# Kernel tuning notes

Hardware: AMD Instinct MI355X
Metric: run time of the kernel (lower is better)

Reference implementation:

```python
import jax, jax.numpy as jnp
import numpy as np
import math

D_MODEL = 1024
NUM_HEADS = 16
B, S = 4, 2048


def setup_inputs() -> dict:
    key = jax.random.key(0)
    ks = jax.random.split(key, 12)
    d = D_MODEL
    sc = 1.0 / math.sqrt(d)
    inp = {
        "q": jax.random.normal(ks[0], (B, S, d), jnp.float32),
        "k": jax.random.normal(ks[1], (B, S, d), jnp.float32),
        "v": jax.random.normal(ks[2], (B, S, d), jnp.float32),
        # causal mask, broadcast over batch and heads
        "mask": jnp.tril(jnp.ones((S, S), bool))[None, None, :, :],
        "Wq": jax.random.normal(ks[3], (d, d), jnp.float32) * sc,
        "bq": jnp.zeros((d,), jnp.float32),
        "Wk": jax.random.normal(ks[4], (d, d), jnp.float32) * sc,
        "bk": jnp.zeros((d,), jnp.float32),
        "Wv": jax.random.normal(ks[5], (d, d), jnp.float32) * sc,
        "bv": jnp.zeros((d,), jnp.float32),
        "Wo": jax.random.normal(ks[6], (d, d), jnp.float32) * sc,
        "bo": jnp.zeros((d,), jnp.float32),
    }
    return inp


def reference(q, k, v, mask, Wq, bq, Wk, bk, Wv, bv, Wo, bo):
    b, s, d = q.shape
    h = NUM_HEADS
    dk = d // h
    # QKV projections, then split heads: [B, H, S, dk]
    def split(x):
        return x.reshape(b, -1, h, dk).transpose(0, 2, 1, 3)
    Q = split(q @ Wq + bq)
    K = split(k @ Wk + bk)
    V = split(v @ Wv + bv)
    scores = jnp.einsum("bhqd,bhkd->bhqk", Q, K) / jnp.sqrt(jnp.float32(dk))
    scores = jnp.where(mask, scores, jnp.float32(-jnp.inf))
    attn = jax.nn.softmax(scores, axis=-1)  # dropout is identity in eval
    ctx = jnp.einsum("bhqk,bhkd->bhqd", attn, V)
    ctx = ctx.transpose(0, 2, 1, 3).reshape(b, -1, d)
    return ctx @ Wo + bo
```

## Files before the change

kernel.cpp:

```cpp
#include <hip/hip_runtime.h>
#include <hip/hip_bf16.h>

typedef unsigned short u16;
typedef __bf16 bf16x8 __attribute__((ext_vector_type(8)));
typedef float f32x4 __attribute__((ext_vector_type(4)));

#define D_MODEL 1024
#define NUM_HEADS 16
#define BATCH 4
#define SEQ 2048
#define DK 64
#define MROWS (BATCH * SEQ)
#define TENS (MROWS * D_MODEL)

#define GLOAD16(gp, lp) __builtin_amdgcn_global_load_lds( \
    (const __attribute__((address_space(1))) void*)(gp), \
    (__attribute__((address_space(3))) void*)(lp), 16, 0, 0)

__device__ inline u16 f2bf(float f) {
    __hip_bfloat16 h = __float2bfloat16(f);
    return *reinterpret_cast<u16*>(&h);
}

__global__ __launch_bounds__(256) void transpose4(
    const float* __restrict__ W0, const float* __restrict__ W1,
    const float* __restrict__ W2, const float* __restrict__ W3,
    u16* __restrict__ dst)
{
    __shared__ u16 tile[32][33];
    const float* in = (blockIdx.z == 0) ? W0 : (blockIdx.z == 1) ? W1
                    : (blockIdx.z == 2) ? W2 : W3;
    u16* out = dst + (size_t)blockIdx.z * (D_MODEL * D_MODEL);
    int x = blockIdx.x * 32 + threadIdx.x;
    int y = blockIdx.y * 32 + threadIdx.y;
    for (int i = 0; i < 32; i += 8)
        tile[threadIdx.y + i][threadIdx.x] = f2bf(in[(size_t)(y + i) * D_MODEL + x]);
    __syncthreads();
    x = blockIdx.y * 32 + threadIdx.x;
    y = blockIdx.x * 32 + threadIdx.y;
    for (int i = 0; i < 32; i += 8)
        out[(size_t)(y + i) * D_MODEL + x] = tile[threadIdx.x][threadIdx.y + i];
}

__global__ __launch_bounds__(256) void cvt_bf16(
    const float* __restrict__ x0, const float* __restrict__ x1,
    u16* __restrict__ dst)
{
    const float* x = blockIdx.z ? x1 : x0;
    u16* o = dst + (size_t)blockIdx.z * TENS;
    size_t i = ((size_t)blockIdx.x * 256 + threadIdx.x) * 8;
    f32x4 a = *(const f32x4*)(x + i);
    f32x4 b = *(const f32x4*)(x + i + 4);
    union { u16 s[8]; uint4 v; } u;
    for (int t = 0; t < 4; t++) { u.s[t] = f2bf(a[t]); u.s[4 + t] = f2bf(b[t]); }
    *(uint4*)(o + i) = u.v;
}

template<bool C_F32>
__global__ __launch_bounds__(256) void gemm_b(
    const u16* __restrict__ A0, const u16* __restrict__ A1,
    const u16* __restrict__ Bt0, const u16* __restrict__ Bt1,
    const float* __restrict__ bias0, const float* __restrict__ bias1,
    void* __restrict__ C0, void* __restrict__ C1)
{
    const int z = blockIdx.z;
    const u16* A    = z ? A1 : A0;
    const u16* Bt   = z ? Bt1 : Bt0;
    const float* bias = z ? bias1 : bias0;
    void* Cp        = z ? C1 : C0;
    const int K = D_MODEL, N = D_MODEL;

    __shared__ __align__(16) u16 As[128 * 32];
    __shared__ __align__(16) u16 Bs[128 * 32];

    const int tid  = threadIdx.x;
    const int lane = tid & 63;
    const int w    = tid >> 6;
    const int wr   = w >> 1, wc = w & 1;
    const int m0   = blockIdx.y * 128;
    const int n0   = blockIdx.x * 128;
    const int col_l = lane & 15;
    const int quad  = lane >> 4;
    const int koff  = quad * 8;

    const f32x4 fz = {0.f, 0.f, 0.f, 0.f};
    f32x4 acc[4][4];
    for (int i = 0; i < 4; i++)
        for (int j = 0; j < 4; j++) acc[i][j] = fz;

    for (int k0 = 0; k0 < K; k0 += 32) {
        __syncthreads();
        for (int i = 0; i < 2; i++) {
            int c   = w * 2 + i;
            int row = c * 16 + (lane >> 2);
            GLOAD16(A  + (size_t)(m0 + row) * K + k0 + (lane & 3) * 8, (char*)As + c * 1024);
            GLOAD16(Bt + (size_t)(n0 + row) * K + k0 + (lane & 3) * 8, (char*)Bs + c * 1024);
        }
        __syncthreads();

        bf16x8 af[4], bfr[4];
        for (int i = 0; i < 4; i++)
            af[i] = *(const bf16x8*)&As[(wr * 64 + i * 16 + col_l) * 32 + koff];
        for (int j = 0; j < 4; j++)
            bfr[j] = *(const bf16x8*)&Bs[(wc * 64 + j * 16 + col_l) * 32 + koff];
        for (int i = 0; i < 4; i++)
            for (int j = 0; j < 4; j++)
                acc[i][j] = __builtin_amdgcn_mfma_f32_16x16x32_bf16(
                    af[i], bfr[j], acc[i][j], 0, 0, 0);
    }

    const int row_q = quad * 4;
    for (int j = 0; j < 4; j++) {
        int colg = n0 + wc * 64 + j * 16 + col_l;
        float bv = bias[colg];
        for (int i = 0; i < 4; i++) {
            int rowg = m0 + wr * 64 + i * 16 + row_q;
            for (int r = 0; r < 4; r++) {
                float val = acc[i][j][r] + bv;
                if (C_F32)
                    ((float*)Cp)[(size_t)(rowg + r) * N + colg] = val;
                else
                    ((u16*)Cp)[(size_t)(rowg + r) * N + colg] = f2bf(val);
            }
        }
    }
}

__global__ __launch_bounds__(256) void attn_kernel(
    const u16* __restrict__ Q, const u16* __restrict__ K,
    const u16* __restrict__ V, u16* __restrict__ ctx)
{
    __shared__ __align__(16) u16 Ksf[64 * 64];
    __shared__ __align__(16) u16 Vts[64 * 64];
    __shared__ __align__(16) u16 Ps[4][16][72];

    const int tid  = threadIdx.x;
    const int lane = tid & 63;
    const int w    = tid >> 6;
    const int bh   = blockIdx.x;
    const int qt   = blockIdx.y;
    const int b    = bh >> 4, h = bh & 15;
    const int q0   = qt * 128;
    const size_t rowbase = (size_t)b * SEQ;
    const int colbase = h * DK;

    const int col_l = lane & 15;
    const int quad  = lane >> 4;
    const int r0 = tid >> 3, cc0 = tid & 7, r1 = r0 + 32;

    bf16x8 aq[2][2];
    for (int rb = 0; rb < 2; rb++) {
        const u16* qp = Q + (rowbase + q0 + rb * 64 + w * 16 + col_l) * D_MODEL + colbase;
        aq[rb][0] = *(const bf16x8*)(qp + quad * 8);
        aq[rb][1] = *(const bf16x8*)(qp + 32 + quad * 8);
    }

    bf16x8 ones;
    for (int i = 0; i < 8; i++) ones[i] = (__bf16)1.0f;

    const f32x4 fz = {0.f, 0.f, 0.f, 0.f};
    f32x4 oacc[2][4];
    for (int rb = 0; rb < 2; rb++)
        for (int j = 0; j < 4; j++) oacc[rb][j] = fz;
    f32x4 lacc[2] = {fz, fz};

    const int ktmax = 2 * qt + 1;
    for (int kt = 0; kt <= ktmax; kt++) {
        const int k0 = kt * 64;
        uint4 vv0 = *(const uint4*)(V + (rowbase + k0 + r0) * D_MODEL + colbase + cc0 * 8);
        uint4 vv1 = *(const uint4*)(V + (rowbase + k0 + r1) * D_MODEL + colbase + cc0 * 8);
        __syncthreads();
        for (int i = 0; i < 2; i++) {
            int c   = w * 2 + i;
            int row = c * 8 + (lane >> 3);
            int bb  = (lane & 7) ^ (row & 7);
            GLOAD16(K + (rowbase + k0 + row) * D_MODEL + colbase + bb * 8,
                    (char*)Ksf + c * 1024);
        }
        {
            union { uint4 v; u16 s[8]; } t0, t1;
            t0.v = vv0; t1.v = vv1;
            int cb0 = r0 ^ (cc0 << 3), cb1 = r1 ^ (cc0 << 3);
            for (int jj = 0; jj < 8; jj++) Vts[(cc0 * 8 + jj) * 64 + cb0] = t0.s[jj];
            for (int jj = 0; jj < 8; jj++) Vts[(cc0 * 8 + jj) * 64 + cb1] = t1.s[jj];
        }
        __syncthreads();

        for (int rb = 0; rb < 2; rb++) {
            if (rb == 0 && kt > 2 * qt) continue;

            f32x4 sacc[4];
            for (int j = 0; j < 4; j++) sacc[j] = fz;
            __builtin_amdgcn_s_setprio(1);
            for (int j = 0; j < 4; j++) {
                int krow = j * 16 + col_l, sw = krow & 7;
                bf16x8 bk0 = *(const bf16x8*)&Ksf[krow * 64 + ((quad ^ sw) * 8)];
                bf16x8 bk1 = *(const bf16x8*)&Ksf[krow * 64 + (((4 + quad) ^ sw) * 8)];
                sacc[j] = __builtin_amdgcn_mfma_f32_16x16x32_bf16(aq[rb][0], bk0, sacc[j], 0, 0, 0);
                sacc[j] = __builtin_amdgcn_mfma_f32_16x16x32_bf16(aq[rb][1], bk1, sacc[j], 0, 0, 0);
            }
            __builtin_amdgcn_s_setprio(0);

            const bool diag = (kt == 2 * qt + rb);
            const int qg = q0 + rb * 64 + w * 16 + quad * 4;
            for (int j = 0; j < 4; j++) {
                int kg = k0 + j * 16 + col_l;
                for (int r = 0; r < 4; r++) {
                    float e = __expf(sacc[j][r] * 0.125f);
                    if (diag && kg > qg + r) e = 0.f;
                    Ps[w][quad * 4 + r][j * 16 + col_l] = f2bf(e);
                }
            }
            __threadfence_block();

            bf16x8 ap0 = *(const bf16x8*)&Ps[w][col_l][quad * 8];
            bf16x8 ap1 = *(const bf16x8*)&Ps[w][col_l][32 + quad * 8];
            __builtin_amdgcn_s_setprio(1);
            lacc[rb] = __builtin_amdgcn_mfma_f32_16x16x32_bf16(ap0, ones, lacc[rb], 0, 0, 0);
            lacc[rb] = __builtin_amdgcn_mfma_f32_16x16x32_bf16(ap1, ones, lacc[rb], 0, 0, 0);
            for (int j = 0; j < 4; j++) {
                int vrow = j * 16 + col_l, sw = (vrow >> 3) & 7;
                bf16x8 bv0 = *(const bf16x8*)&Vts[vrow * 64 + ((quad ^ sw) * 8)];
                bf16x8 bv1 = *(const bf16x8*)&Vts[vrow * 64 + (((4 + quad) ^ sw) * 8)];
                oacc[rb][j] = __builtin_amdgcn_mfma_f32_16x16x32_bf16(ap0, bv0, oacc[rb][j], 0, 0, 0);
                oacc[rb][j] = __builtin_amdgcn_mfma_f32_16x16x32_bf16(ap1, bv1, oacc[rb][j], 0, 0, 0);
            }
            __builtin_amdgcn_s_setprio(0);
        }
    }

    for (int rb = 0; rb < 2; rb++) {
        for (int r = 0; r < 4; r++) {
            float inv = 1.f / lacc[rb][r];
            int rowg = q0 + rb * 64 + w * 16 + quad * 4 + r;
            for (int j = 0; j < 4; j++)
                ctx[(rowbase + rowg) * D_MODEL + colbase + j * 16 + col_l] =
                    f2bf(oacc[rb][j][r] * inv);
        }
    }
}

extern "C" void kernel_launch(void* const* d_in, const int* in_sizes, int n_in,
                              void* d_out, int out_size, void* d_ws, size_t ws_size,
                              hipStream_t stream) {
    const float* q  = (const float*)d_in[0];
    const float* k  = (const float*)d_in[1];
    const float* v  = (const float*)d_in[2];
    const float* Wq = (const float*)d_in[4];
    const float* bq = (const float*)d_in[5];
    const float* Wk = (const float*)d_in[6];
    const float* bk = (const float*)d_in[7];
    const float* Wv = (const float*)d_in[8];
    const float* bv = (const float*)d_in[9];
    const float* Wo = (const float*)d_in[10];
    const float* bo = (const float*)d_in[11];

    char* ws = (char*)d_ws;
    u16* Qb  = (u16*)(ws + (0ull  << 20));
    u16* Kb  = (u16*)(ws + (16ull << 20));
    u16* Vb  = (u16*)(ws + (32ull << 20));
    u16* WT  = (u16*)(ws + (48ull << 20));
    u16* WqT = WT + 0ull * D_MODEL * D_MODEL;
    u16* WkT = WT + 1ull * D_MODEL * D_MODEL;
    u16* WvT = WT + 2ull * D_MODEL * D_MODEL;
    u16* WoT = WT + 3ull * D_MODEL * D_MODEL;
    u16* ctx = Qb;
    u16* s0  = (u16*)d_out;
    u16* s1  = s0 + (size_t)TENS;

    transpose4<<<dim3(32, 32, 4), dim3(32, 8), 0, stream>>>(Wq, Wk, Wv, Wo, WT);

    const int cvt_blocks = TENS / (256 * 8);
    dim3 gg(D_MODEL / 128, MROWS / 128);

    cvt_bf16<<<dim3(cvt_blocks, 1, 2), 256, 0, stream>>>(q, k, s0);
    gemm_b<false><<<dim3(gg.x, gg.y, 2), 256, 0, stream>>>(
        s0, s1, WqT, WkT, bq, bk, Qb, Kb);

    cvt_bf16<<<dim3(cvt_blocks, 1, 1), 256, 0, stream>>>(v, v, s0);
    gemm_b<false><<<dim3(gg.x, gg.y, 1), 256, 0, stream>>>(
        s0, s0, WvT, WvT, bv, bv, Vb, Vb);

    attn_kernel<<<dim3(BATCH * NUM_HEADS, SEQ / 128), 256, 0, stream>>>(Qb, Kb, Vb, ctx);

    gemm_b<true><<<dim3(gg.x, gg.y, 1), 256, 0, stream>>>(
        ctx, ctx, WoT, WoT, bo, bo, d_out, d_out);
}
```

Measured before the change: 395.8 us.

## Prefetch next K/V tile into registers, rebalance causal tile order, refine V swizzle

Loads the next K and V tiles into registers one iteration ahead, replacing the direct global-to-LDS K load and the per-iteration V load, so global latency overlaps with the current tile's MFMA work. The query-tile index is remapped so heavy and light causal tiles are interleaved across blocks, which balances the workload. The V transpose swizzle gains an extra XOR term to cut LDS bank conflicts on the scatter writes, and the causal mask test is skipped on non-diagonal tiles. In exchange it uses more registers and makes a redundant load on the last iteration, and the grid mapping assumes the y dimension is 16.

```diff
diff --git a/kernel.cpp b/kernel.cpp
--- a/kernel.cpp
+++ b/kernel.cpp
@@ -138,7 +138,10 @@
     const int lane = tid & 63;
     const int w    = tid >> 6;
     const int bh   = blockIdx.x;
-    const int qt   = blockIdx.y;
+    const int iy = blockIdx.y;
+    const int sj = iy >> 2, jj4 = iy & 3;
+    const int qt = (sj == 0) ? jj4 : (sj == 1) ? 15 - jj4
+                 : (sj == 2) ? 7 - jj4 : 8 + jj4;
     const int b    = bh >> 4, h = bh & 15;
     const int q0   = qt * 128;
     const size_t rowbase = (size_t)b * SEQ;
@@ -147,6 +150,16 @@
     const int col_l = lane & 15;
     const int quad  = lane >> 4;
     const int r0 = tid >> 3, cc0 = tid & 7, r1 = r0 + 32;
+
+    const int c0 = w * 2, c1 = c0 + 1;
+    const int krow0 = c0 * 8 + (lane >> 3), krow1 = c1 * 8 + (lane >> 3);
+    const int bb0 = (lane & 7) ^ (krow0 & 7), bb1 = (lane & 7) ^ (krow1 & 7);
+    const u16* Kg0 = K + (rowbase + krow0) * D_MODEL + colbase + bb0 * 8;
+    const u16* Kg1 = K + (rowbase + krow1) * D_MODEL + colbase + bb1 * 8;
+    u16* KsW0 = &Ksf[c0 * 512 + lane * 8];
+    u16* KsW1 = &Ksf[c1 * 512 + lane * 8];
+    const u16* Vg0 = V + (rowbase + r0) * D_MODEL + colbase + cc0 * 8;
+    const u16* Vg1 = V + (rowbase + r1) * D_MODEL + colbase + cc0 * 8;
 
     bf16x8 aq[2][2];
     for (int rb = 0; rb < 2; rb++) {
@@ -165,26 +178,37 @@
     f32x4 lacc[2] = {fz, fz};
 
     const int ktmax = 2 * qt + 1;
+    const size_t tstep = (size_t)64 * D_MODEL;
+
+    uint4 kA0 = *(const uint4*)Kg0;
+    uint4 kA1 = *(const uint4*)Kg1;
+    uint4 vA0 = *(const uint4*)Vg0;
+    uint4 vA1 = *(const uint4*)Vg1;
+
     for (int kt = 0; kt <= ktmax; kt++) {
         const int k0 = kt * 64;
-        uint4 vv0 = *(const uint4*)(V + (rowbase + k0 + r0) * D_MODEL + colbase + cc0 * 8);
-        uint4 vv1 = *(const uint4*)(V + (rowbase + k0 + r1) * D_MODEL + colbase + cc0 * 8);
-        __syncthreads();
-        for (int i = 0; i < 2; i++) {
-            int c   = w * 2 + i;
-            int row = c * 8 + (lane >> 3);
-            int bb  = (lane & 7) ^ (row & 7);
-            GLOAD16(K + (rowbase + k0 + row) * D_MODEL + colbase + bb * 8,
-                    (char*)Ksf + c * 1024);
-        }
+        const size_t noff = (size_t)((kt < ktmax) ? kt + 1 : ktmax) * tstep;
+        uint4 kB0 = *(const uint4*)(Kg0 + noff);
+        uint4 kB1 = *(const uint4*)(Kg1 + noff);
+        uint4 vB0 = *(const uint4*)(Vg0 + noff);
+        uint4 vB1 = *(const uint4*)(Vg1 + noff);
+
+        asm volatile("s_waitcnt lgkmcnt(0)" ::: "memory");
+        __builtin_amdgcn_s_barrier();
+
+        *(uint4*)KsW0 = kA0;
+        *(uint4*)KsW1 = kA1;
         {
             union { uint4 v; u16 s[8]; } t0, t1;
-            t0.v = vv0; t1.v = vv1;
-            int cb0 = r0 ^ (cc0 << 3), cb1 = r1 ^ (cc0 << 3);
-            for (int jj = 0; jj < 8; jj++) Vts[(cc0 * 8 + jj) * 64 + cb0] = t0.s[jj];
-            for (int jj = 0; jj < 8; jj++) Vts[(cc0 * 8 + jj) * 64 + cb1] = t1.s[jj];
-        }
-        __syncthreads();
+            t0.v = vA0; t1.v = vA1;
+            for (int jj = 0; jj < 8; jj++) {
+                int fx = ((cc0 ^ jj) & 7) << 3;
+                Vts[(cc0 * 8 + jj) * 64 + (r0 ^ fx)] = t0.s[jj];
+                Vts[(cc0 * 8 + jj) * 64 + (r1 ^ fx)] = t1.s[jj];
+            }
+        }
+        asm volatile("s_waitcnt lgkmcnt(0)" ::: "memory");
+        __builtin_amdgcn_s_barrier();
 
         for (int rb = 0; rb < 2; rb++) {
             if (rb == 0 && kt > 2 * qt) continue;
@@ -202,14 +226,21 @@
             __builtin_amdgcn_s_setprio(0);
 
             const bool diag = (kt == 2 * qt + rb);
-            const int qg = q0 + rb * 64 + w * 16 + quad * 4;
-            for (int j = 0; j < 4; j++) {
-                int kg = k0 + j * 16 + col_l;
-                for (int r = 0; r < 4; r++) {
-                    float e = __expf(sacc[j][r] * 0.125f);
-                    if (diag && kg > qg + r) e = 0.f;
-                    Ps[w][quad * 4 + r][j * 16 + col_l] = f2bf(e);
+            if (diag) {
+                const int qg = q0 + rb * 64 + w * 16 + quad * 4;
+                for (int j = 0; j < 4; j++) {
+                    int kg = k0 + j * 16 + col_l;
+                    for (int r = 0; r < 4; r++) {
+                        float e = __expf(sacc[j][r] * 0.125f);
+                        if (kg > qg + r) e = 0.f;
+                        Ps[w][quad * 4 + r][j * 16 + col_l] = f2bf(e);
+                    }
                 }
+            } else {
+                for (int j = 0; j < 4; j++)
+                    for (int r = 0; r < 4; r++)
+                        Ps[w][quad * 4 + r][j * 16 + col_l] =
+                            f2bf(__expf(sacc[j][r] * 0.125f));
             }
             __threadfence_block();
 
@@ -219,7 +250,7 @@
             lacc[rb] = __builtin_amdgcn_mfma_f32_16x16x32_bf16(ap0, ones, lacc[rb], 0, 0, 0);
             lacc[rb] = __builtin_amdgcn_mfma_f32_16x16x32_bf16(ap1, ones, lacc[rb], 0, 0, 0);
             for (int j = 0; j < 4; j++) {
-                int vrow = j * 16 + col_l, sw = (vrow >> 3) & 7;
+                int vrow = j * 16 + col_l, sw = ((vrow >> 3) ^ vrow) & 7;
                 bf16x8 bv0 = *(const bf16x8*)&Vts[vrow * 64 + ((quad ^ sw) * 8)];
                 bf16x8 bv1 = *(const bf16x8*)&Vts[vrow * 64 + (((4 + quad) ^ sw) * 8)];
                 oacc[rb][j] = __builtin_amdgcn_mfma_f32_16x16x32_bf16(ap0, bv0, oacc[rb][j], 0, 0, 0);
@@ -227,6 +258,8 @@
             }
             __builtin_amdgcn_s_setprio(0);
         }
+
+        kA0 = kB0; kA1 = kB1; vA0 = vB0; vA1 = vB1;
     }
 
     for (int rb = 0; rb < 2; rb++) {
```

Measured after the change: 362.5 us. -8.4%, faster.
